# Optimization experiments

Measured on AMD Instinct MI355X. Metric: run time of the kernel, lower is better.

Reference implementation:

```python
import jax, jax.numpy as jnp
import numpy as np

B, S, H, V = 32, 512, 1024, 250002


def setup_inputs() -> dict:
    key = jax.random.key(0)
    k1, k2, k3 = jax.random.split(key, 3)
    hidden_states = jax.random.normal(k1, (B, S, H), dtype=jnp.float32)
    input_ids = jax.random.randint(k2, (B, S), 0, V, dtype=jnp.int32)
    attention_mask = jnp.ones((B, S), dtype=jnp.float32)
    W = jax.random.normal(k3, (1, H), dtype=jnp.float32) * (1.0 / np.sqrt(H))
    b = jnp.zeros((1,), dtype=jnp.float32)
    return {"hidden_states": hidden_states, "input_ids": input_ids,
            "attention_mask": attention_mask, "W": W, "b": b}


def reference(hidden_states, input_ids, attention_mask, W, b):
    # linear(hidden,1).squeeze(-1): [B,S]
    token_weights = jnp.einsum('bsh,h->bs', hidden_states, W[0]) + b[0]
    token_weights = token_weights * attention_mask
    token_weights = jax.nn.relu(token_weights)
    # scatter-add each token weight into its vocab bin, per batch row.
    # Flatten (batch, token_id) -> single segment id so one segment_sum handles all rows.
    flat_ids = (input_ids + V * jnp.arange(B, dtype=input_ids.dtype)[:, None]).reshape(-1)
    sparse_embedding = jax.ops.segment_sum(
        token_weights.reshape(-1), flat_ids, num_segments=B * V)
    return sparse_embedding.reshape(B, V)
```

## Files before the change

kernel.cpp:

```cpp
#include <hip/hip_runtime.h>
#include <hip/hip_bf16.h>

#define BB 32
#define SS 512
#define HH 1024
#define VV 250002

__global__ __launch_bounds__(256) void sparse_head_kernel(
    const float* __restrict__ hidden,
    const int* __restrict__ ids,
    const float* __restrict__ mask,
    const float* __restrict__ W,
    const float* __restrict__ bias,
    float* __restrict__ out)
{
    const int wave_in_block = threadIdx.x >> 6;
    const int lane = threadIdx.x & 63;
    const int token = blockIdx.x * (blockDim.x >> 6) + wave_in_block;
    if (token >= BB * SS) return;

    const float4* __restrict__ h4 = reinterpret_cast<const float4*>(hidden + (size_t)token * HH);
    const float4* __restrict__ w4 = reinterpret_cast<const float4*>(W);

    float sum = 0.0f;
#pragma unroll
    for (int i = 0; i < 4; ++i) {
        const float4 hv = h4[i * 64 + lane];
        const float4 wv = w4[i * 64 + lane];
        sum = fmaf(hv.x, wv.x, sum);
        sum = fmaf(hv.y, wv.y, sum);
        sum = fmaf(hv.z, wv.z, sum);
        sum = fmaf(hv.w, wv.w, sum);
    }

#pragma unroll
    for (int off = 32; off > 0; off >>= 1)
        sum += __shfl_xor(sum, off, 64);

    if (lane == 0) {
        float tw = (sum + bias[0]) * mask[token];
        tw = fmaxf(tw, 0.0f);
        if (tw != 0.0f) {
            const int b = token / SS;
            const int id = ids[token];
            atomicAdd(&out[(size_t)b * VV + id], tw);
        }
    }
}

extern "C" void kernel_launch(void* const* d_in, const int* in_sizes, int n_in,
                              void* d_out, int out_size, void* d_ws, size_t ws_size,
                              hipStream_t stream) {
    const float* hidden = (const float*)d_in[0];
    const int*   ids    = (const int*)d_in[1];
    const float* mask   = (const float*)d_in[2];
    const float* W      = (const float*)d_in[3];
    const float* bias   = (const float*)d_in[4];
    float* out = (float*)d_out;

    hipMemsetAsync(out, 0, (size_t)out_size * sizeof(float), stream);

    const int tokens = BB * SS;
    const int waves_per_block = 4;
    const int blocks = tokens / waves_per_block;
    sparse_head_kernel<<<blocks, 256, 0, stream>>>(hidden, ids, mask, W, bias, out);
}
```

Measured before the change: 23.24 us.

## Fuse output zeroing into dot kernel and split scatter into separate pass

Replaces the hipMemsetAsync with nontemporal zero stores done inside the dot-product kernel. Token weights now go to a workspace buffer, and a second kernel performs the atomic scatter once zeroing is complete. Each wave handles two tokens over a fixed grid of 2048 blocks. This removes the separate memset launch and overlaps the 32MB output clear with the 64MB hidden-state read. In exchange it adds a second kernel launch and a workspace round trip.

```diff
diff --git a/kernel.cpp b/kernel.cpp
--- a/kernel.cpp
+++ b/kernel.cpp
@@ -5,46 +5,71 @@
 #define SS 512
 #define HH 1024
 #define VV 250002
+#define TOKENS (BB * SS)
+#define OUT_FLOATS (BB * VV)
+#define OUT_F4 (OUT_FLOATS / 4)
 
-__global__ __launch_bounds__(256) void sparse_head_kernel(
+#define K1_BLOCKS 2048
+#define K1_THREADS 256
+
+typedef float floatx4 __attribute__((ext_vector_type(4)));
+
+__global__ __launch_bounds__(K1_THREADS) void k1_zero_and_dot(
     const float* __restrict__ hidden,
-    const int* __restrict__ ids,
     const float* __restrict__ mask,
     const float* __restrict__ W,
     const float* __restrict__ bias,
+    float* __restrict__ out,
+    float* __restrict__ tw_ws)
+{
+    const int tid = blockIdx.x * K1_THREADS + threadIdx.x;
+    const int lane = threadIdx.x & 63;
+    const int wave_global = tid >> 6;
+
+    const float4* __restrict__ w4 = reinterpret_cast<const float4*>(W);
+    const float bias0 = bias[0];
+
+#pragma unroll
+    for (int tt = 0; tt < 2; ++tt) {
+        const int token = wave_global * 2 + tt;
+        const float4* __restrict__ h4 =
+            reinterpret_cast<const float4*>(hidden + (size_t)token * HH);
+        float sum = 0.0f;
+#pragma unroll
+        for (int i = 0; i < 4; ++i) {
+            const float4 hv = h4[i * 64 + lane];
+            const float4 wv = w4[i * 64 + lane];
+            sum = fmaf(hv.x, wv.x, sum);
+            sum = fmaf(hv.y, wv.y, sum);
+            sum = fmaf(hv.z, wv.z, sum);
+            sum = fmaf(hv.w, wv.w, sum);
+        }
+#pragma unroll
+        for (int off = 32; off > 0; off >>= 1)
+            sum += __shfl_xor(sum, off, 64);
+        if (lane == 0) {
+            const float tw = fmaxf((sum + bias0) * mask[token], 0.0f);
+            tw_ws[token] = tw;
+        }
+    }
+
+    floatx4* __restrict__ o4 = reinterpret_cast<floatx4*>(out);
+    const floatx4 z = {0.f, 0.f, 0.f, 0.f};
+    for (int i = tid; i < OUT_F4; i += K1_BLOCKS * K1_THREADS)
+        __builtin_nontemporal_store(z, &o4[i]);
+}
+
+__global__ __launch_bounds__(256) void k2_scatter(
+    const float* __restrict__ tw_ws,
+    const int* __restrict__ ids,
     float* __restrict__ out)
 {
-    const int wave_in_block = threadIdx.x >> 6;
-    const int lane = threadIdx.x & 63;
-    const int token = blockIdx.x * (blockDim.x >> 6) + wave_in_block;
-    if (token >= BB * SS) return;
-
-    const float4* __restrict__ h4 = reinterpret_cast<const float4*>(hidden + (size_t)token * HH);
-    const float4* __restrict__ w4 = reinterpret_cast<const float4*>(W);
-
-    float sum = 0.0f;
-#pragma unroll
-    for (int i = 0; i < 4; ++i) {
-        const float4 hv = h4[i * 64 + lane];
-        const float4 wv = w4[i * 64 + lane];
-        sum = fmaf(hv.x, wv.x, sum);
-        sum = fmaf(hv.y, wv.y, sum);
-        sum = fmaf(hv.z, wv.z, sum);
-        sum = fmaf(hv.w, wv.w, sum);
-    }
-
-#pragma unroll
-    for (int off = 32; off > 0; off >>= 1)
-        sum += __shfl_xor(sum, off, 64);
-
-    if (lane == 0) {
-        float tw = (sum + bias[0]) * mask[token];
-        tw = fmaxf(tw, 0.0f);
-        if (tw != 0.0f) {
-            const int b = token / SS;
-            const int id = ids[token];
-            atomicAdd(&out[(size_t)b * VV + id], tw);
-        }
+    const int t = blockIdx.x * 256 + threadIdx.x;
+    if (t >= TOKENS) return;
+    const float tw = tw_ws[t];
+    if (tw != 0.0f) {
+        const int b = t / SS;
+        atomicAdd(&out[(size_t)b * VV + ids[t]], tw);
     }
 }
 
@@ -56,12 +81,9 @@
     const float* mask   = (const float*)d_in[2];
     const float* W      = (const float*)d_in[3];
     const float* bias   = (const float*)d_in[4];
-    float* out = (float*)d_out;
+    float* out   = (float*)d_out;
+    float* tw_ws = (float*)d_ws;
 
-    hipMemsetAsync(out, 0, (size_t)out_size * sizeof(float), stream);
-
-    const int tokens = BB * SS;
-    const int waves_per_block = 4;
-    const int blocks = tokens / waves_per_block;
-    sparse_head_kernel<<<blocks, 256, 0, stream>>>(hidden, ids, mask, W, bias, out);
+    k1_zero_and_dot<<<K1_BLOCKS, K1_THREADS, 0, stream>>>(hidden, mask, W, bias, out, tw_ws);
+    k2_scatter<<<(TOKENS + 255) / 256, 256, 0, stream>>>(tw_ws, ids, out);
 }
```

Result: faster. 21.69 us (-6.6%).

## Replace memset with nontemporal zero kernel and process two tokens per wave

Applied to the files above, without the earlier changes.

Swaps hipMemsetAsync for a custom grid-stride kernel that zeroes the output with nontemporal vector stores. The dot/scatter kernel now has each wavefront handle two tokens. All hidden-state and weight loads are issued up front, so more memory requests are in flight and the W loads and bias read are shared across two tokens. The cost is more registers per thread and a fixed grid size tied to the token count.

```diff
diff --git a/kernel.cpp b/kernel.cpp
--- a/kernel.cpp
+++ b/kernel.cpp
@@ -5,8 +5,26 @@
 #define SS 512
 #define HH 1024
 #define VV 250002
+#define TOKENS (BB * SS)
+#define OUT_FLOATS (BB * VV)
+#define OUT_F4 (OUT_FLOATS / 4)
 
-__global__ __launch_bounds__(256) void sparse_head_kernel(
+typedef float floatx4 __attribute__((ext_vector_type(4)));
+
+#define Z_BLOCKS 2048
+#define Z_THREADS 256
+__global__ __launch_bounds__(Z_THREADS) void k1_zero(float* __restrict__ out)
+{
+    const int tid = blockIdx.x * Z_THREADS + threadIdx.x;
+    floatx4* __restrict__ o4 = reinterpret_cast<floatx4*>(out);
+    const floatx4 z = {0.f, 0.f, 0.f, 0.f};
+    for (int i = tid; i < OUT_F4; i += Z_BLOCKS * Z_THREADS)
+        __builtin_nontemporal_store(z, &o4[i]);
+}
+
+#define D_BLOCKS 2048
+#define D_THREADS 256
+__global__ __launch_bounds__(D_THREADS) void k2_dot_scatter(
     const float* __restrict__ hidden,
     const int* __restrict__ ids,
     const float* __restrict__ mask,
@@ -14,37 +32,49 @@
     const float* __restrict__ bias,
     float* __restrict__ out)
 {
-    const int wave_in_block = threadIdx.x >> 6;
+    const int tid = blockIdx.x * D_THREADS + threadIdx.x;
     const int lane = threadIdx.x & 63;
-    const int token = blockIdx.x * (blockDim.x >> 6) + wave_in_block;
-    if (token >= BB * SS) return;
+    const int wave = tid >> 6;
 
-    const float4* __restrict__ h4 = reinterpret_cast<const float4*>(hidden + (size_t)token * HH);
     const float4* __restrict__ w4 = reinterpret_cast<const float4*>(W);
+    const float bias0 = bias[0];
 
-    float sum = 0.0f;
+    const float4* __restrict__ h4a =
+        reinterpret_cast<const float4*>(hidden + (size_t)(wave * 2 + 0) * HH);
+    const float4* __restrict__ h4b =
+        reinterpret_cast<const float4*>(hidden + (size_t)(wave * 2 + 1) * HH);
+
+    float4 ha[4], hb[4], wv[4];
+#pragma unroll
+    for (int i = 0; i < 4; ++i) ha[i] = h4a[i * 64 + lane];
+#pragma unroll
+    for (int i = 0; i < 4; ++i) hb[i] = h4b[i * 64 + lane];
+#pragma unroll
+    for (int i = 0; i < 4; ++i) wv[i] = w4[i * 64 + lane];
+
+    float sa = 0.f, sb = 0.f;
 #pragma unroll
     for (int i = 0; i < 4; ++i) {
-        const float4 hv = h4[i * 64 + lane];
-        const float4 wv = w4[i * 64 + lane];
-        sum = fmaf(hv.x, wv.x, sum);
-        sum = fmaf(hv.y, wv.y, sum);
-        sum = fmaf(hv.z, wv.z, sum);
-        sum = fmaf(hv.w, wv.w, sum);
+        sa = fmaf(ha[i].x, wv[i].x, sa); sa = fmaf(ha[i].y, wv[i].y, sa);
+        sa = fmaf(ha[i].z, wv[i].z, sa); sa = fmaf(ha[i].w, wv[i].w, sa);
+        sb = fmaf(hb[i].x, wv[i].x, sb); sb = fmaf(hb[i].y, wv[i].y, sb);
+        sb = fmaf(hb[i].z, wv[i].z, sb); sb = fmaf(hb[i].w, wv[i].w, sb);
     }
 
 #pragma unroll
-    for (int off = 32; off > 0; off >>= 1)
-        sum += __shfl_xor(sum, off, 64);
+    for (int off = 32; off > 0; off >>= 1) {
+        sa += __shfl_xor(sa, off, 64);
+        sb += __shfl_xor(sb, off, 64);
+    }
 
     if (lane == 0) {
-        float tw = (sum + bias[0]) * mask[token];
-        tw = fmaxf(tw, 0.0f);
-        if (tw != 0.0f) {
-            const int b = token / SS;
-            const int id = ids[token];
-            atomicAdd(&out[(size_t)b * VV + id], tw);
-        }
+        const int t0 = wave * 2;
+        const float twa = fmaxf((sa + bias0) * mask[t0], 0.0f);
+        const float twb = fmaxf((sb + bias0) * mask[t0 + 1], 0.0f);
+        if (twa != 0.0f)
+            atomicAdd(&out[(size_t)(t0 / SS) * VV + ids[t0]], twa);
+        if (twb != 0.0f)
+            atomicAdd(&out[(size_t)((t0 + 1) / SS) * VV + ids[t0 + 1]], twb);
     }
 }
 
@@ -58,10 +88,6 @@
     const float* bias   = (const float*)d_in[4];
     float* out = (float*)d_out;
 
-    hipMemsetAsync(out, 0, (size_t)out_size * sizeof(float), stream);
-
-    const int tokens = BB * SS;
-    const int waves_per_block = 4;
-    const int blocks = tokens / waves_per_block;
-    sparse_head_kernel<<<blocks, 256, 0, stream>>>(hidden, ids, mask, W, bias, out);
+    k1_zero<<<Z_BLOCKS, Z_THREADS, 0, stream>>>(out);
+    k2_dot_scatter<<<D_BLOCKS, D_THREADS, 0, stream>>>(hidden, ids, mask, W, bias, out);
 }
```

Result: no change. 23.61 us (+1.6%).
